# Optimization experiments

Hardware: AMD Instinct MI355X
Metric: run time of the kernel (lower is better)

Reference implementation:

```python
import jax, jax.numpy as jnp
import numpy as np

N_IN, N_UP, N_OUT = 65536, 262144, 131072
C_IN, C_OUT = 128, 64
K1, K2, K3 = 27, 27, 16      # kernel offsets: 3x3x3x1, 3x3x3x1, 2x2x2x2
M1, M2, M3 = 65536, 131072, 131072  # gather/scatter pairs per offset
EPS = 1e-6
ALPHA = 0.0


def setup_inputs() -> dict:
    key = jax.random.key(0)
    ks = jax.random.split(key, 13)
    return {
        "input_feats": jax.random.normal(ks[0], (N_IN, C_IN), jnp.float32),
        "encoder_feats": jax.random.normal(ks[1], (N_UP, C_OUT), jnp.float32),
        "W1t": jax.random.normal(ks[2], (K1, C_IN, C_OUT), jnp.float32) * 0.05,
        "W2": jax.random.normal(ks[3], (K2, C_OUT, C_OUT), jnp.float32) * 0.05,
        "W3": jax.random.normal(ks[4], (K3, C_OUT, C_OUT), jnp.float32) * 0.05,
        "Wp": jax.random.normal(ks[5], (C_OUT, 1), jnp.float32) * 0.05,
        "bp": jnp.zeros((1,), jnp.float32),
        "kin1": jax.random.randint(ks[6], (K1, M1), 0, N_IN, jnp.int32),
        "kout1": jax.random.randint(ks[7], (K1, M1), 0, N_UP, jnp.int32),
        "kin2": jax.random.randint(ks[8], (K2, M2), 0, N_UP, jnp.int32),
        "kout2": jax.random.randint(ks[9], (K2, M2), 0, N_UP, jnp.int32),
        "kin3": jax.random.randint(ks[10], (K3, M3), 0, N_UP, jnp.int32),
        "kout3": jax.random.randint(ks[11], (K3, M3), 0, N_OUT, jnp.int32),
        "n_out": N_OUT,
    }


def _sparse_conv(x, W, kin, kout, n_out):
    """Kernel-map gather-GEMM-scatter sparse conv.
    x: [N_in, Cin]; W: [K, Cin, Cout]; kin/kout: [K, M] index pairs."""
    y = jnp.einsum('kmc,kcd->kmd', x[kin], W)  # gather + per-offset GEMM
    out = jnp.zeros((n_out, W.shape[-1]), x.dtype)
    return out.at[kout].add(y)                 # scatter-accumulate


def _inorm(x):
    # MinkowskiInstanceNorm, single batch instance: per-channel over points
    mu = x.mean(0, keepdims=True)
    var = x.var(0, keepdims=True)
    return (x - mu) * jax.lax.rsqrt(var + EPS)


def reference(input_feats, encoder_feats, W1t, W2, W3, Wp, bp,
              kin1, kout1, kin2, kout2, kin3, kout3, n_out):
    n_up = encoder_feats.shape[0]
    # dec_block_1: gen conv-transpose 3x3x3x1 s2 -> IN -> ELU -> conv 3x3x3x1 -> IN -> ELU
    x = _sparse_conv(input_feats, W1t, kin1, kout1, n_up)
    x = jax.nn.elu(_inorm(x))
    x = _sparse_conv(x, W2, kin2, kout2, n_up)
    x = jax.nn.elu(_inorm(x))
    # skip connection
    x = x + encoder_feats
    # dec_block_2: conv k=2 stride [1,1,1,2] -> IN -> ELU
    x = _sparse_conv(x, W3, kin3, kout3, n_out)
    x = jax.nn.elu(_inorm(x))
    # 1x1 pruning conv (bias=True) + threshold keep mask
    pruning = x @ Wp + bp                      # [N_OUT, 1]
    keep = pruning[:, 0] > ALPHA
    # MinkowskiPruning gathers kept rows (dynamic shape); static-shape
    # equivalent: zero out pruned rows and return the mask.
    return x * keep[:, None].astype(x.dtype), keep
```

## Files before the change

### kernel.cpp

```cpp
#include <hip/hip_runtime.h>
#include <math.h>

#define N_IN   65536
#define N_UP   262144
#define N_OUT  131072
#define C_IN   128
#define C_OUT  64
#define K1     27
#define K2     27
#define K3     16
#define M1     65536
#define M2     131072
#define M3     131072
#define EPSV   1e-6f
#define WPK    256
#define WPK_SHIFT 8

template <int CIN, int MSHIFT>
__global__ __launch_bounds__(256) void conv_gemm(
    const float* __restrict__ X, const float* __restrict__ W,
    const int* __restrict__ kin, const int* __restrict__ kout,
    float* __restrict__ outp)
{
    __shared__ float lds_t[4][64][20];
    __shared__ int   lds_dst[4][64];

    const int lane = threadIdx.x & 63;
    const int wv   = threadIdx.x >> 6;
    const int wave = blockIdx.x * 4 + wv;
    const int k    = __builtin_amdgcn_readfirstlane(wave >> WPK_SHIFT);
    const int widx = wave & (WPK - 1);
    constexpr int R  = (1 << MSHIFT) / WPK;
    constexpr int NB = R / 64;
    constexpr int KC = CIN / 16;

    const float* Wk = W + (size_t)k * (CIN * 64);
    const int base = (k << MSHIFT) + widx * R;

    for (int b = 0; b < NB; ++b) {
        const int j   = base + b * 64 + lane;
        const int src = kin[j];
        const int dst = kout[j];
        lds_dst[wv][lane] = dst;

        const float4* xr = (const float4*)(X + (size_t)src * CIN);

        float acc[64];
#pragma unroll
        for (int c = 0; c < 64; ++c) acc[c] = 0.f;

        float4 xa0 = xr[0], xa1 = xr[1], xa2 = xr[2], xa3 = xr[3];

        for (int kc = 0; kc < KC; ++kc) {
            float4 xb0, xb1, xb2, xb3;
            if (kc + 1 < KC) {
                xb0 = xr[(kc + 1) * 4 + 0];
                xb1 = xr[(kc + 1) * 4 + 1];
                xb2 = xr[(kc + 1) * 4 + 2];
                xb3 = xr[(kc + 1) * 4 + 3];
            }
            float xs[16];
            xs[0]=xa0.x; xs[1]=xa0.y; xs[2]=xa0.z; xs[3]=xa0.w;
            xs[4]=xa1.x; xs[5]=xa1.y; xs[6]=xa1.z; xs[7]=xa1.w;
            xs[8]=xa2.x; xs[9]=xa2.y; xs[10]=xa2.z; xs[11]=xa2.w;
            xs[12]=xa3.x; xs[13]=xa3.y; xs[14]=xa3.z; xs[15]=xa3.w;

            const float* wrow = Wk + kc * 16 * 64;
#pragma unroll
            for (int i = 0; i < 16; ++i) {
                const float xi = xs[i];
                const float* wr = wrow + i * 64;
#pragma unroll
                for (int c = 0; c < 64; ++c)
                    acc[c] = fmaf(xi, wr[c], acc[c]);
            }
            xa0 = xb0; xa1 = xb1; xa2 = xb2; xa3 = xb3;
        }

#pragma unroll
        for (int cc = 0; cc < 4; ++cc) {
#pragma unroll
            for (int q = 0; q < 4; ++q) {
                float4 v;
                v.x = acc[cc * 16 + q * 4 + 0];
                v.y = acc[cc * 16 + q * 4 + 1];
                v.z = acc[cc * 16 + q * 4 + 2];
                v.w = acc[cc * 16 + q * 4 + 3];
                *(float4*)&lds_t[wv][lane][q * 4] = v;
            }
            const int c16 = lane & 15;
#pragma unroll
            for (int t = 0; t < 16; ++t) {
                const int rr = (lane >> 4) + 4 * t;
                const float v = lds_t[wv][rr][c16];
                const int   d = lds_dst[wv][rr];
                atomicAdd(outp + (size_t)d * 64 + cc * 16 + c16, v);
            }
        }
    }
}

__global__ __launch_bounds__(256) void stats_kernel(
    const float* __restrict__ x, int nrows, float* __restrict__ stats)
{
    __shared__ float sh[2][4][64];
    const int c  = threadIdx.x & 63;
    const int rw = threadIdx.x >> 6;
    float s = 0.f, s2 = 0.f;
    for (int r = blockIdx.x * 4 + rw; r < nrows; r += gridDim.x * 4) {
        float v = x[(size_t)r * 64 + c];
        s += v;
        s2 = fmaf(v, v, s2);
    }
    sh[0][rw][c] = s;
    sh[1][rw][c] = s2;
    __syncthreads();
    if (rw == 0) {
        s  = (sh[0][0][c] + sh[0][1][c]) + (sh[0][2][c] + sh[0][3][c]);
        s2 = (sh[1][0][c] + sh[1][1][c]) + (sh[1][2][c] + sh[1][3][c]);
        atomicAdd(stats + c, s);
        atomicAdd(stats + 64 + c, s2);
    }
}

__global__ void finalize_stats(float* stats, float inv_n)
{
    const int c = threadIdx.x;
    float mu  = stats[c] * inv_n;
    float var = stats[64 + c] * inv_n - mu * mu;
    stats[128 + c] = mu;
    stats[192 + c] = rsqrtf(var + EPSV);
}

__global__ __launch_bounds__(256) void norm_elu(
    float* __restrict__ x, const float* __restrict__ stats,
    const float* __restrict__ enc)
{
    const int i = blockIdx.x * 256 + threadIdx.x;
    const int c = i & 63;
    float v = (x[i] - stats[128 + c]) * stats[192 + c];
    v = (v > 0.f) ? v : expm1f(v);
    if (enc) v += enc[i];
    x[i] = v;
}

__global__ __launch_bounds__(256) void final_kernel(
    const float* __restrict__ x, const float* __restrict__ stats,
    const float* __restrict__ Wp, const float* __restrict__ bp,
    float* __restrict__ outp)
{
    const int lane = threadIdx.x & 63;
    const int wid  = threadIdx.x >> 6;
    const int row  = blockIdx.x * 4 + wid;

    float v = (x[(size_t)row * 64 + lane] - stats[128 + lane]) * stats[192 + lane];
    v = (v > 0.f) ? v : expm1f(v);

    float p = v * Wp[lane];
#pragma unroll
    for (int m = 1; m < 64; m <<= 1)
        p += __shfl_xor(p, m, 64);
    p += bp[0];

    const bool keep = p > 0.0f;
    outp[(size_t)row * 64 + lane] = keep ? v : 0.f;
    if (lane == 0)
        outp[(size_t)N_OUT * 64 + row] = keep ? 1.f : 0.f;
}

extern "C" void kernel_launch(void* const* d_in, const int* in_sizes, int n_in,
                              void* d_out, int out_size, void* d_ws, size_t ws_size,
                              hipStream_t stream)
{
    const float* in_feats = (const float*)d_in[0];
    const float* enc      = (const float*)d_in[1];
    const float* W1       = (const float*)d_in[2];
    const float* W2       = (const float*)d_in[3];
    const float* W3       = (const float*)d_in[4];
    const float* Wp       = (const float*)d_in[5];
    const float* bp       = (const float*)d_in[6];
    const int* kin1  = (const int*)d_in[7];
    const int* kout1 = (const int*)d_in[8];
    const int* kin2  = (const int*)d_in[9];
    const int* kout2 = (const int*)d_in[10];
    const int* kin3  = (const int*)d_in[11];
    const int* kout3 = (const int*)d_in[12];
    float* outp = (float*)d_out;

    char* ws = (char*)d_ws;
    float* up_a   = (float*)ws;
    float* up_b   = (float*)(ws + 67108864);
    float* out3   = up_a;
    float* statsA = (float*)(ws + 134217728);
    float* statsB = statsA + 256;
    float* statsC = statsA + 512;

    hipMemsetAsync(up_a, 0, (size_t)N_UP * 64 * 4, stream);
    hipMemsetAsync(up_b, 0, (size_t)N_UP * 64 * 4, stream);
    hipMemsetAsync(statsA, 0, 3 * 256 * 4, stream);

    conv_gemm<128, 16><<<(K1 * WPK) / 4, 256, 0, stream>>>(
        in_feats, W1, kin1, kout1, up_a);
    stats_kernel<<<512, 256, 0, stream>>>(up_a, N_UP, statsA);
    finalize_stats<<<1, 64, 0, stream>>>(statsA, 1.f / N_UP);
    norm_elu<<<(N_UP * 64) / 256, 256, 0, stream>>>(up_a, statsA, nullptr);

    conv_gemm<64, 17><<<(K2 * WPK) / 4, 256, 0, stream>>>(
        up_a, W2, kin2, kout2, up_b);
    stats_kernel<<<512, 256, 0, stream>>>(up_b, N_UP, statsB);
    finalize_stats<<<1, 64, 0, stream>>>(statsB, 1.f / N_UP);
    norm_elu<<<(N_UP * 64) / 256, 256, 0, stream>>>(up_b, statsB, enc);

    hipMemsetAsync(out3, 0, (size_t)N_OUT * 64 * 4, stream);
    conv_gemm<64, 17><<<(K3 * WPK) / 4, 256, 0, stream>>>(
        up_b, W3, kin3, kout3, out3);
    stats_kernel<<<512, 256, 0, stream>>>(out3, N_OUT, statsC);
    finalize_stats<<<1, 64, 0, stream>>>(statsC, 1.f / N_OUT);

    final_kernel<<<N_OUT / 4, 256, 0, stream>>>(out3, statsC, Wp, bp, outp);
}
```

Baseline: 2.505 ms.

## Sort kernel map by output row and accumulate convs in LDS with fixed-point

Builds a CSR of gather pairs by output row (histogram, scan, scatter) each conv, then each block owns 128 output rows and accumulates GEMM results into LDS with integer fixed-point atomics, writing rows once. Per-channel stats are fused into the conv epilogue using 64-bit fixed-point global atomics, and the memsets and stats kernels are dropped. This removes global float atomics and output zeroing, at the cost of extra sorting passes, LDS pressure, a capped bucket size (BCAP) that can silently drop entries, and quantization error.

```diff
diff --git a/kernel.cpp b/kernel.cpp
--- a/kernel.cpp
+++ b/kernel.cpp
@@ -4,45 +4,146 @@
 #define N_IN   65536
 #define N_UP   262144
 #define N_OUT  131072
-#define C_IN   128
-#define C_OUT  64
 #define K1     27
 #define K2     27
 #define K3     16
-#define M1     65536
-#define M2     131072
-#define M3     131072
+#define KM1    (27 * 65536)
+#define KM2    (27 * 131072)
+#define KM3    (16 * 131072)
 #define EPSV   1e-6f
-#define WPK    256
-#define WPK_SHIFT 8
-
-template <int CIN, int MSHIFT>
-__global__ __launch_bounds__(256) void conv_gemm(
+#define BROWS  128
+#define BCAP   3584
+#define QSCALE 4194304.0f
+#define QINV   (1.0f / 4194304.0f)
+#define SSCALE 1048576.0
+
+typedef unsigned long long u64;
+
+
+__global__ __launch_bounds__(256) void hist_kernel(
+    const int* __restrict__ kout, int km, int* __restrict__ counts)
+{
+    for (int j = blockIdx.x * 256 + threadIdx.x; j < km; j += gridDim.x * 256)
+        atomicAdd(&counts[kout[j]], 1);
+}
+
+__global__ __launch_bounds__(256) void scan_partial(
+    int* __restrict__ a, int* __restrict__ bsums)
+{
+    __shared__ int sa[256], sb[256];
+    const int t = threadIdx.x;
+    int4 v = ((const int4*)a)[blockIdx.x * 256 + t];
+    const int s = v.x + v.y + v.z + v.w;
+    sa[t] = s; __syncthreads();
+    int* src = sa; int* dst = sb;
+    for (int off = 1; off < 256; off <<= 1) {
+        dst[t] = (t >= off) ? src[t - off] + src[t] : src[t];
+        __syncthreads();
+        int* tmp = src; src = dst; dst = tmp;
+    }
+    const int incl = src[t];
+    const int excl = incl - s;
+    int4 o;
+    o.x = excl; o.y = excl + v.x; o.z = o.y + v.y; o.w = o.z + v.z;
+    ((int4*)a)[blockIdx.x * 256 + t] = o;
+    if (t == 255) bsums[blockIdx.x] = incl;
+}
+
+__global__ void scan_top(int* __restrict__ bsums, int nb)
+{
+    __shared__ int sa[256], sb[256];
+    const int t = threadIdx.x;
+    const int s = (t < nb) ? bsums[t] : 0;
+    sa[t] = s; __syncthreads();
+    int* src = sa; int* dst = sb;
+    for (int off = 1; off < 256; off <<= 1) {
+        dst[t] = (t >= off) ? src[t - off] + src[t] : src[t];
+        __syncthreads();
+        int* tmp = src; src = dst; dst = tmp;
+    }
+    if (t < nb) bsums[t] = src[t] - s;
+}
+
+__global__ __launch_bounds__(256) void add_off(
+    int* __restrict__ rs, const int* __restrict__ bsums,
+    int* __restrict__ cursor, int n, int km)
+{
+    const int i = blockIdx.x * 256 + threadIdx.x;
+    const int v = rs[i] + bsums[i >> 10];
+    rs[i] = v; cursor[i] = v;
+    if (i == 0) rs[n] = km;
+}
+
+__global__ __launch_bounds__(256) void scatter_kernel(
+    const int* __restrict__ kin, const int* __restrict__ kout,
+    int* __restrict__ cursor, unsigned* __restrict__ sorted,
+    int km, int mshift)
+{
+    for (int j = blockIdx.x * 256 + threadIdx.x; j < km; j += gridDim.x * 256) {
+        const int pos = atomicAdd(&cursor[kout[j]], 1);
+        sorted[pos] = (unsigned)kin[j] | ((unsigned)(j >> mshift) << 18);
+    }
+}
+
+
+template <int CIN, int K>
+__global__ __launch_bounds__(256) void conv_sorted(
     const float* __restrict__ X, const float* __restrict__ W,
-    const int* __restrict__ kin, const int* __restrict__ kout,
-    float* __restrict__ outp)
-{
-    __shared__ float lds_t[4][64][20];
-    __shared__ int   lds_dst[4][64];
-
-    const int lane = threadIdx.x & 63;
-    const int wv   = threadIdx.x >> 6;
-    const int wave = blockIdx.x * 4 + wv;
-    const int k    = __builtin_amdgcn_readfirstlane(wave >> WPK_SHIFT);
-    const int widx = wave & (WPK - 1);
-    constexpr int R  = (1 << MSHIFT) / WPK;
-    constexpr int NB = R / 64;
+    const int* __restrict__ rowst, const unsigned* __restrict__ sorted,
+    float* __restrict__ outp, u64* __restrict__ stats_i)
+{
+    __shared__ int      y[BROWS * 65];
+    __shared__ unsigned bkt[BCAP];
+    __shared__ int      rs[BROWS + 1];
+    __shared__ int      bc[28], bs[28], bcur[28], fpre[29], qpre[29];
+    __shared__ float    sred[256], sred2[256];
+
+    const int t    = threadIdx.x;
+    const int lane = t & 63;
+    const int wv   = t >> 6;
+    const int r0   = blockIdx.x * BROWS;
+
+    for (int i = t; i < BROWS * 65; i += 256) y[i] = 0;
+    if (t < 28) bc[t] = 0;
+    if (t <= BROWS) rs[t] = rowst[r0 + t];
+    __syncthreads();
+
+    const int p0 = rs[0], p1 = rs[BROWS];
+
+    for (int p = p0 + t; p < p1; p += 256)
+        atomicAdd(&bc[sorted[p] >> 18], 1);
+    __syncthreads();
+    if (t == 0) {
+        int run = 0, fr = 0, qr = 0;
+        for (int k = 0; k < K; ++k) {
+            bs[k] = run; bcur[k] = run; run += bc[k];
+            fpre[k] = fr; fr += bc[k] >> 6;
+            qpre[k] = qr; qr += ((bc[k] & 63) + 15) >> 4;
+        }
+        fpre[K] = fr; qpre[K] = qr;
+    }
+    __syncthreads();
+    for (int p = p0 + t; p < p1; p += 256) {
+        const unsigned e = sorted[p];
+        const int k = e >> 18;
+        int lo = 0, hi = BROWS;
+        while (hi - lo > 1) { const int mid = (lo + hi) >> 1; if (rs[mid] <= p) lo = mid; else hi = mid; }
+        const int pos = atomicAdd(&bcur[k], 1);
+        if (pos < BCAP) bkt[pos] = (e & 0x3FFFFu) | ((unsigned)lo << 18);
+    }
+    __syncthreads();
+
     constexpr int KC = CIN / 16;
 
-    const float* Wk = W + (size_t)k * (CIN * 64);
-    const int base = (k << MSHIFT) + widx * R;
-
-    for (int b = 0; b < NB; ++b) {
-        const int j   = base + b * 64 + lane;
-        const int src = kin[j];
-        const int dst = kout[j];
-        lds_dst[wv][lane] = dst;
-
+    const int nf = fpre[K];
+    for (int fb = wv; fb < nf; fb += 4) {
+        int lo = 0, hi = K;
+        while (hi - lo > 1) { const int mid = (lo + hi) >> 1; if (fpre[mid] <= fb) lo = mid; else hi = mid; }
+        const int k = lo, b = fb - fpre[k];
+        const unsigned e = bkt[bs[k] + b * 64 + lane];
+        const int src = e & 0x3FFFFu;
+        const int ld  = e >> 18;
+        const float* Wk = W + (size_t)k * (CIN * 64);
         const float4* xr = (const float4*)(X + (size_t)src * CIN);
 
         float acc[64];
@@ -77,83 +178,107 @@
             xa0 = xb0; xa1 = xb1; xa2 = xb2; xa3 = xb3;
         }
 
-#pragma unroll
-        for (int cc = 0; cc < 4; ++cc) {
-#pragma unroll
-            for (int q = 0; q < 4; ++q) {
-                float4 v;
-                v.x = acc[cc * 16 + q * 4 + 0];
-                v.y = acc[cc * 16 + q * 4 + 1];
-                v.z = acc[cc * 16 + q * 4 + 2];
-                v.w = acc[cc * 16 + q * 4 + 3];
-                *(float4*)&lds_t[wv][lane][q * 4] = v;
-            }
-            const int c16 = lane & 15;
-#pragma unroll
-            for (int t = 0; t < 16; ++t) {
-                const int rr = (lane >> 4) + 4 * t;
-                const float v = lds_t[wv][rr][c16];
-                const int   d = lds_dst[wv][rr];
-                atomicAdd(outp + (size_t)d * 64 + cc * 16 + c16, v);
+        int* yr = &y[ld * 65];
+#pragma unroll
+        for (int c = 0; c < 64; ++c)
+            atomicAdd(&yr[c], (int)rintf(acc[c] * QSCALE));
+    }
+
+    const int nq = qpre[K];
+    const int cq = lane >> 4;
+    for (int qb = wv; qb < nq; qb += 4) {
+        int lo = 0, hi = K;
+        while (hi - lo > 1) { const int mid = (lo + hi) >> 1; if (qpre[mid] <= qb) lo = mid; else hi = mid; }
+        const int k = lo, tq = qb - qpre[k];
+        const int tbase = bs[k] + (bc[k] & ~63);
+        const int tcnt  = bc[k] & 63;
+        const int ei = tq * 16 + (lane & 15);
+        const bool valid = ei < tcnt;
+        const unsigned e = valid ? bkt[tbase + ei] : 0u;
+        const int src = e & 0x3FFFFu;
+        const int ld  = e >> 18;
+        const float4* x4 = (const float4*)(X + (size_t)src * CIN);
+        const float*  wq = W + (size_t)k * (CIN * 64) + cq * 16;
+        const float4  z4 = make_float4(0.f, 0.f, 0.f, 0.f);
+
+        float acc[16];
+#pragma unroll
+        for (int c = 0; c < 16; ++c) acc[c] = 0.f;
+
+        for (int i4 = 0; i4 < CIN / 4; ++i4) {
+            const float4 xv = valid ? x4[i4] : z4;
+            const float xs4[4] = { xv.x, xv.y, xv.z, xv.w };
+#pragma unroll
+            for (int j = 0; j < 4; ++j) {
+                const float xi = xs4[j];
+                const float* wr = wq + (i4 * 4 + j) * 64;
+#pragma unroll
+                for (int c = 0; c < 16; ++c)
+                    acc[c] = fmaf(xi, wr[c], acc[c]);
             }
         }
-    }
-}
-
-__global__ __launch_bounds__(256) void stats_kernel(
-    const float* __restrict__ x, int nrows, float* __restrict__ stats)
-{
-    __shared__ float sh[2][4][64];
-    const int c  = threadIdx.x & 63;
-    const int rw = threadIdx.x >> 6;
+        if (valid) {
+            int* yr = &y[ld * 65 + cq * 16];
+#pragma unroll
+            for (int c = 0; c < 16; ++c)
+                atomicAdd(&yr[c], (int)rintf(acc[c] * QSCALE));
+        }
+    }
+    __syncthreads();
+
     float s = 0.f, s2 = 0.f;
-    for (int r = blockIdx.x * 4 + rw; r < nrows; r += gridDim.x * 4) {
-        float v = x[(size_t)r * 64 + c];
-        s += v;
-        s2 = fmaf(v, v, s2);
-    }
-    sh[0][rw][c] = s;
-    sh[1][rw][c] = s2;
-    __syncthreads();
-    if (rw == 0) {
-        s  = (sh[0][0][c] + sh[0][1][c]) + (sh[0][2][c] + sh[0][3][c]);
-        s2 = (sh[1][0][c] + sh[1][1][c]) + (sh[1][2][c] + sh[1][3][c]);
-        atomicAdd(stats + c, s);
-        atomicAdd(stats + 64 + c, s2);
-    }
-}
-
-__global__ void finalize_stats(float* stats, float inv_n)
+    for (int i = t; i < BROWS * 64; i += 256) {
+        const int row = i >> 6, c = i & 63;
+        const float v = (float)y[row * 65 + c] * QINV;
+        outp[(size_t)(r0 + row) * 64 + c] = v;
+        s += v; s2 = fmaf(v, v, s2);
+    }
+    sred[t] = s; sred2[t] = s2;
+    __syncthreads();
+    if (t < 64) {
+        s  = (sred[t] + sred[t + 64]) + (sred[t + 128] + sred[t + 192]);
+        s2 = (sred2[t] + sred2[t + 64]) + (sred2[t + 128] + sred2[t + 192]);
+        const long long qs  = llrint((double)s  * SSCALE);
+        const long long qs2 = llrint((double)s2 * SSCALE);
+        atomicAdd(&stats_i[t],      (u64)qs);
+        atomicAdd(&stats_i[64 + t], (u64)qs2);
+    }
+}
+
+
+__global__ void finalize_stats(const u64* __restrict__ si,
+                               float* __restrict__ sf, double inv_n)
 {
     const int c = threadIdx.x;
-    float mu  = stats[c] * inv_n;
-    float var = stats[64 + c] * inv_n - mu * mu;
-    stats[128 + c] = mu;
-    stats[192 + c] = rsqrtf(var + EPSV);
+    const double sum  = (double)(long long)si[c]      * (1.0 / SSCALE);
+    const double sum2 = (double)(long long)si[64 + c] * (1.0 / SSCALE);
+    const double mu   = sum * inv_n;
+    const double var  = sum2 * inv_n - mu * mu;
+    sf[c]      = (float)mu;
+    sf[64 + c] = rsqrtf((float)(var + (double)EPSV));
 }
 
 __global__ __launch_bounds__(256) void norm_elu(
-    float* __restrict__ x, const float* __restrict__ stats,
+    float* __restrict__ x, const float* __restrict__ sf,
     const float* __restrict__ enc)
 {
     const int i = blockIdx.x * 256 + threadIdx.x;
     const int c = i & 63;
-    float v = (x[i] - stats[128 + c]) * stats[192 + c];
+    float v = (x[i] - sf[c]) * sf[64 + c];
     v = (v > 0.f) ? v : expm1f(v);
     if (enc) v += enc[i];
     x[i] = v;
 }
 
 __global__ __launch_bounds__(256) void final_kernel(
-    const float* __restrict__ x, const float* __restrict__ stats,
+    const float* __restrict__ x, const float* __restrict__ sf,
     const float* __restrict__ Wp, const float* __restrict__ bp,
     float* __restrict__ outp)
 {
     const int lane = threadIdx.x & 63;
-    const int wid  = threadIdx.x >> 6;
-    const int row  = blockIdx.x * 4 + wid;
-
-    float v = (x[(size_t)row * 64 + lane] - stats[128 + lane]) * stats[192 + lane];
+    const int row  = blockIdx.x * 4 + (threadIdx.x >> 6);
+
+    float v = (x[(size_t)row * 64 + lane] - sf[lane]) * sf[64 + lane];
     v = (v > 0.f) ? v : expm1f(v);
 
     float p = v * Wp[lane];
@@ -167,6 +292,7 @@
     if (lane == 0)
         outp[(size_t)N_OUT * 64 + row] = keep ? 1.f : 0.f;
 }
+
 
 extern "C" void kernel_launch(void* const* d_in, const int* in_sizes, int n_in,
                               void* d_out, int out_size, void* d_ws, size_t ws_size,
@@ -188,34 +314,53 @@
     float* outp = (float*)d_out;
 
     char* ws = (char*)d_ws;
-    float* up_a   = (float*)ws;
-    float* up_b   = (float*)(ws + 67108864);
-    float* out3   = up_a;
-    float* statsA = (float*)(ws + 134217728);
-    float* statsB = statsA + 256;
-    float* statsC = statsA + 512;
-
-    hipMemsetAsync(up_a, 0, (size_t)N_UP * 64 * 4, stream);
-    hipMemsetAsync(up_b, 0, (size_t)N_UP * 64 * 4, stream);
-    hipMemsetAsync(statsA, 0, 3 * 256 * 4, stream);
-
-    conv_gemm<128, 16><<<(K1 * WPK) / 4, 256, 0, stream>>>(
-        in_feats, W1, kin1, kout1, up_a);
-    stats_kernel<<<512, 256, 0, stream>>>(up_a, N_UP, statsA);
-    finalize_stats<<<1, 64, 0, stream>>>(statsA, 1.f / N_UP);
-    norm_elu<<<(N_UP * 64) / 256, 256, 0, stream>>>(up_a, statsA, nullptr);
-
-    conv_gemm<64, 17><<<(K2 * WPK) / 4, 256, 0, stream>>>(
-        up_a, W2, kin2, kout2, up_b);
-    stats_kernel<<<512, 256, 0, stream>>>(up_b, N_UP, statsB);
-    finalize_stats<<<1, 64, 0, stream>>>(statsB, 1.f / N_UP);
-    norm_elu<<<(N_UP * 64) / 256, 256, 0, stream>>>(up_b, statsB, enc);
-
-    hipMemsetAsync(out3, 0, (size_t)N_OUT * 64 * 4, stream);
-    conv_gemm<64, 17><<<(K3 * WPK) / 4, 256, 0, stream>>>(
-        up_b, W3, kin3, kout3, out3);
-    stats_kernel<<<512, 256, 0, stream>>>(out3, N_OUT, statsC);
-    finalize_stats<<<1, 64, 0, stream>>>(statsC, 1.f / N_OUT);
-
-    final_kernel<<<N_OUT / 4, 256, 0, stream>>>(out3, statsC, Wp, bp, outp);
-}
+    float*    up_a  = (float*)ws;
+    float*    up_b  = (float*)(ws + 67108864);
+    float*    out3  = up_a;
+    u64*      siA   = (u64*)(ws + 134217728);
+    u64*      siB   = (u64*)(ws + 134219776);
+    u64*      siC   = (u64*)(ws + 134221824);
+    float*    sfA   = (float*)(ws + 134223872);
+    float*    sfB   = sfA + 128;
+    float*    sfC   = sfA + 256;
+    int*      rs    = (int*)(ws + 134230016);
+    int*      cur   = (int*)(ws + 135282688);
+    int*      bsums = (int*)(ws + 136331264);
+    unsigned* sorted = (unsigned*)(ws + 136335360);
+
+    hipMemsetAsync(siA, 0, 3 * 2048, stream);
+
+    hipMemsetAsync(rs, 0, (N_UP + 1) * 4, stream);
+    hist_kernel<<<1024, 256, 0, stream>>>(kout1, KM1, rs);
+    scan_partial<<<N_UP / 1024, 256, 0, stream>>>(rs, bsums);
+    scan_top<<<1, 256, 0, stream>>>(bsums, N_UP / 1024);
+    add_off<<<N_UP / 256, 256, 0, stream>>>(rs, bsums, cur, N_UP, KM1);
+    scatter_kernel<<<1024, 256, 0, stream>>>(kin1, kout1, cur, sorted, KM1, 16);
+    conv_sorted<128, K1><<<N_UP / BROWS, 256, 0, stream>>>(
+        in_feats, W1, rs, sorted, up_a, siA);
+    finalize_stats<<<1, 64, 0, stream>>>(siA, sfA, 1.0 / N_UP);
+    norm_elu<<<(N_UP * 64) / 256, 256, 0, stream>>>(up_a, sfA, nullptr);
+
+    hipMemsetAsync(rs, 0, (N_UP + 1) * 4, stream);
+    hist_kernel<<<1024, 256, 0, stream>>>(kout2, KM2, rs);
+    scan_partial<<<N_UP / 1024, 256, 0, stream>>>(rs, bsums);
+    scan_top<<<1, 256, 0, stream>>>(bsums, N_UP / 1024);
+    add_off<<<N_UP / 256, 256, 0, stream>>>(rs, bsums, cur, N_UP, KM2);
+    scatter_kernel<<<1024, 256, 0, stream>>>(kin2, kout2, cur, sorted, KM2, 17);
+    conv_sorted<64, K2><<<N_UP / BROWS, 256, 0, stream>>>(
+        up_a, W2, rs, sorted, up_b, siB);
+    finalize_stats<<<1, 64, 0, stream>>>(siB, sfB, 1.0 / N_UP);
+    norm_elu<<<(N_UP * 64) / 256, 256, 0, stream>>>(up_b, sfB, enc);
+
+    hipMemsetAsync(rs, 0, (N_OUT + 1) * 4, stream);
+    hist_kernel<<<1024, 256, 0, stream>>>(kout3, KM3, rs);
+    scan_partial<<<N_OUT / 1024, 256, 0, stream>>>(rs, bsums);
+    scan_top<<<1, 256, 0, stream>>>(bsums, N_OUT / 1024);
+    add_off<<<N_OUT / 256, 256, 0, stream>>>(rs, bsums, cur, N_OUT, KM3);
+    scatter_kernel<<<1024, 256, 0, stream>>>(kin3, kout3, cur, sorted, KM3, 17);
+    conv_sorted<64, K3><<<N_OUT / BROWS, 256, 0, stream>>>(
+        up_b, W3, rs, sorted, out3, siC);
+    finalize_stats<<<1, 64, 0, stream>>>(siC, sfC, 1.0 / N_OUT);
+
+    final_kernel<<<N_OUT / 4, 256, 0, stream>>>(out3, sfC, Wp, bp, outp);
+}
```

Measured after the change: 8.453 ms. +237.4%, slower.
